# Kernel optimization log

Measured on AMD Instinct MI355X. Metric: run time of the kernel, lower is better.

The kernel has to match this reference:

```python
import jax, jax.numpy as jnp
import numpy as np

EMBED = 1024
HEADS = 16


def setup_inputs() -> dict:
    key = jax.random.key(0)
    k1, k2, k3 = jax.random.split(key, 3)
    B, S, D = 2, 2048, EMBED
    x = jax.random.normal(k1, (B, S, D), dtype=jnp.float32)
    # nn.Linear weights: stored as [out, in]; y = x @ W.T
    w_qkv = jax.random.normal(k2, (3 * D, D), dtype=jnp.float32) * (D ** -0.5)
    w_out = jax.random.normal(k3, (D, D), dtype=jnp.float32) * (D ** -0.5)
    return {"x": x, "w_qkv": w_qkv, "w_out": w_out}


def reference(x, w_qkv, w_out):
    B, S, D = x.shape
    H = HEADS
    hd = D // H
    qkv = x @ w_qkv.T                       # [B, S, 3D]
    q, k, v = jnp.split(qkv, 3, axis=-1)
    # 'b l (head k) -> b head l k'
    def heads(t):
        return t.reshape(B, S, H, hd).transpose(0, 2, 1, 3)
    q, k, v = heads(q), heads(k), heads(v)
    scale = hd ** 0.5
    scores = jnp.einsum('bhqd,bhkd->bhqk', q, k) / scale
    probs = jax.nn.softmax(scores, axis=-1)
    out = jnp.einsum('bhqk,bhkd->bhqd', probs, v)  # [B, H, S, hd]
    out = out.transpose(0, 2, 1, 3).reshape(B, S, D)
    return out @ w_out.T
```

## Files before the change

kernel.cpp:

```cpp
#include <hip/hip_runtime.h>

typedef short short8 __attribute__((ext_vector_type(8)));
typedef short short4v __attribute__((ext_vector_type(4)));
typedef float floatx4 __attribute__((ext_vector_type(4)));
typedef unsigned short ushort_t;

#define EMBED 1024
#define HEADS 16
#define HD 64
#define SEQ 2048
#define BATCH 2
#define QSCALE 0.18033688f

__device__ inline ushort_t f2bf(float f) {
    unsigned int u = __float_as_uint(f);
    u += 0x7fff + ((u >> 16) & 1);
    return (ushort_t)(u >> 16);
}

typedef const __attribute__((address_space(1))) unsigned int* gas_t;
typedef __attribute__((address_space(3))) unsigned int* las_t;
__device__ inline void async_copy16(const ushort_t* g, ushort_t* l) {
    __builtin_amdgcn_global_load_lds((gas_t)g, (las_t)l, 16, 0, 0);
}

__global__ void cast3_kernel(const float* __restrict__ a, ushort_t* __restrict__ oa, int na,
                             const float* __restrict__ b, ushort_t* __restrict__ ob, int nb,
                             const float* __restrict__ c, ushort_t* __restrict__ oc, int nc) {
    int idx = (blockIdx.x * blockDim.x + threadIdx.x) * 4;
    const float* in; ushort_t* out;
    if (idx < na)            { in = a;  out = oa; }
    else if (idx < na + nb)  { in = b;  out = ob; idx -= na; }
    else if (idx < na + nb + nc) { in = c; out = oc; idx -= na + nb; }
    else return;
    float4 f = *(const float4*)(in + idx);
    ushort4 o;
    o.x = f2bf(f.x); o.y = f2bf(f.y); o.z = f2bf(f.z); o.w = f2bf(f.w);
    *(ushort4*)(out + idx) = o;
}

#define BM 128
#define BN 128
#define BK 64

template<int MODE>
__launch_bounds__(256, 3)
__global__ void gemm_bt(const ushort_t* __restrict__ A, const ushort_t* __restrict__ B,
                        float* __restrict__ outF,
                        ushort_t* __restrict__ qb, ushort_t* __restrict__ kb,
                        ushort_t* __restrict__ vtb,
                        int M, int N, int K) {
    __shared__ ushort_t As[BM * BK];
    __shared__ ushort_t Bs[BN * BK];
    const int id   = blockIdx.x;
    const int jj   = id >> 3;
    const int bm   = (id & 7) * 4 + (jj & 3);
    const int bn   = jj >> 2;
    const int t    = threadIdx.x;
    const int lane = t & 63;
    const int wave = t >> 6;
    const int wm   = (wave >> 1) * 64;
    const int wn   = (wave & 1) * 64;
    const int m0   = bm * BM;
    const int n0   = bn * BN;
    const int col  = lane & 15;
    const int quad = lane >> 4;

    const int srow = lane >> 3;
    const int sgr  = (lane & 7) ^ (srow & 7);
    const int slot0 = quad ^ (col & 7);

    floatx4 acc[4][4] = {};

    for (int k0 = 0; k0 < K; k0 += BK) {
        for (int half = 0; half < 4; ++half) {
            int row0 = wave * 32 + half * 8;
            int r = row0 + srow;
            async_copy16(A + (size_t)(m0 + r) * K + k0 + sgr * 8, &As[row0 * BK]);
            async_copy16(B + (size_t)(n0 + r) * K + k0 + sgr * 8, &Bs[row0 * BK]);
        }
        __syncthreads();
        short8 a[2][4], b[2][4];
        for (int i = 0; i < 4; ++i) {
            int base = (wm + i * 16 + col) * BK;
            a[0][i] = *(const short8*)(&As[base + slot0 * 8]);
            a[1][i] = *(const short8*)(&As[base + (slot0 ^ 4) * 8]);
        }
        for (int j = 0; j < 4; ++j) {
            int base = (wn + j * 16 + col) * BK;
            b[0][j] = *(const short8*)(&Bs[base + slot0 * 8]);
            b[1][j] = *(const short8*)(&Bs[base + (slot0 ^ 4) * 8]);
        }
        for (int kk = 0; kk < 2; ++kk)
            for (int i = 0; i < 4; ++i)
                for (int j = 0; j < 4; ++j)
                    acc[i][j] = __builtin_amdgcn_mfma_f32_16x16x32_bf16(a[kk][i], b[kk][j], acc[i][j], 0, 0, 0);
        __syncthreads();
    }

    for (int i = 0; i < 4; ++i)
        for (int j = 0; j < 4; ++j) {
            int n = n0 + wn + j * 16 + col;
            int mb = m0 + wm + i * 16 + quad * 4;
            if (MODE == 1) {
                for (int r = 0; r < 4; ++r)
                    outF[(size_t)(mb + r) * N + n] = acc[i][j][r];
            } else {
                int part = n >> 10;
                int within = n & 1023;
                int h = within >> 6, d = within & 63;
                int bb = mb >> 11, s = mb & 2047;
                if (part == 2) {
                    short4v pv;
                    pv.x = (short)f2bf(acc[i][j][0]); pv.y = (short)f2bf(acc[i][j][1]);
                    pv.z = (short)f2bf(acc[i][j][2]); pv.w = (short)f2bf(acc[i][j][3]);
                    *(short4v*)(vtb + (((size_t)bb * HEADS + h) * HD + d) * SEQ + s) = pv;
                } else {
                    ushort_t* dst = (part == 0) ? qb : kb;
                    const float scl = (part == 0) ? QSCALE : 1.0f;
                    for (int r = 0; r < 4; ++r)
                        dst[(((size_t)bb * HEADS + h) * SEQ + s + r) * HD + d] = f2bf(acc[i][j][r] * scl);
                }
            }
        }
}

__launch_bounds__(512, 4)
__global__ void attn_kernel(const ushort_t* __restrict__ qb_, const ushort_t* __restrict__ kb,
                            const ushort_t* __restrict__ vtb, ushort_t* __restrict__ attn) {
    __shared__ __align__(16) ushort_t lds[32768];
    const int id   = blockIdx.x;
    const int jj   = id >> 3;
    const int bh   = (id & 7) * 4 + (jj >> 4);
    const int qblk = jj & 15;
    const int t    = threadIdx.x;
    const int lane = t & 63;
    const int wave = t >> 6;
    const int g    = wave >> 2;
    const int wv   = wave & 3;
    const int col  = lane & 15;
    const int quad = lane >> 4;
    const int q0   = qblk * 128 + wv * 32;
    const int sw   = col & 7;
    const int srow = lane >> 3;
    const int sgr  = lane & 7;

    const ushort_t* Q  = qb_ + (size_t)bh * SEQ * HD;
    const ushort_t* Kp = kb  + (size_t)bh * SEQ * HD;
    const ushort_t* Vt = vtb + (size_t)bh * HD * SEQ;

    ushort_t* Kb0 = &lds[g * 8192];
    ushort_t* Vb0 = &lds[16384 + g * 8192];

    auto stage = [&](int c, int buf) {
        int kt = c << 6;
        #pragma unroll
        for (int inst = 0; inst < 2; ++inst) {
            int row0 = wv * 16 + inst * 8;
            int r = row0 + srow;
            async_copy16(Kp + (size_t)(kt + r) * HD + (sgr ^ (r & 7)) * 8,
                         Kb0 + buf * 4096 + row0 * 64);
            async_copy16(Vt + (size_t)r * SEQ + kt + (sgr ^ (r & 7)) * 8,
                         Vb0 + buf * 4096 + row0 * 64);
        }
    };

    short8 qf[2][2];
    #pragma unroll
    for (int qt = 0; qt < 2; ++qt) {
        qf[qt][0] = *(const short8*)(Q + (size_t)(q0 + qt * 16 + col) * HD + quad * 8);
        qf[qt][1] = *(const short8*)(Q + (size_t)(q0 + qt * 16 + col) * HD + 32 + quad * 8);
    }

    floatx4 acc[2][4] = {};
    float lsum[2] = {0.f, 0.f};

    stage(g, 0);
    __syncthreads();

    for (int i = 0; i < 16; ++i) {
        const int cur = i & 1;
        if (i < 15) stage(2 * (i + 1) + g, cur ^ 1);
        const ushort_t* Kc = Kb0 + cur * 4096;
        const ushort_t* Vc = Vb0 + cur * 4096;

        #pragma unroll
        for (int h = 0; h < 2; ++h) {
            short8 kf[2][2];
            short4v vf[4][2];
            #pragma unroll
            for (int nl = 0; nl < 2; ++nl) {
                int row = (2 * h + nl) * 16 + col;
                kf[nl][0] = *(const short8*)(Kc + row * 64 + ((quad ^ sw) * 8));
                kf[nl][1] = *(const short8*)(Kc + row * 64 + (((4 + quad) ^ sw) * 8));
            }
            #pragma unroll
            for (int dt = 0; dt < 4; ++dt)
                #pragma unroll
                for (int kl = 0; kl < 2; ++kl) {
                    int ks = h * 2 + kl;
                    int row = dt * 16 + col;
                    int slot = (ks * 2 + (quad >> 1)) ^ sw;
                    vf[dt][kl] = *(const short4v*)(Vc + row * 64 + slot * 8 + (quad & 1) * 4);
                }
            #pragma unroll
            for (int qt = 0; qt < 2; ++qt)
                #pragma unroll
                for (int nl = 0; nl < 2; ++nl) {
                    floatx4 z = {};
                    z = __builtin_amdgcn_mfma_f32_16x16x32_bf16(kf[nl][0], qf[qt][0], z, 0, 0, 0);
                    z = __builtin_amdgcn_mfma_f32_16x16x32_bf16(kf[nl][1], qf[qt][1], z, 0, 0, 0);
                    unsigned u0 = __float_as_uint(__builtin_amdgcn_exp2f(z[0]));
                    unsigned u1 = __float_as_uint(__builtin_amdgcn_exp2f(z[1]));
                    unsigned u2 = __float_as_uint(__builtin_amdgcn_exp2f(z[2]));
                    unsigned u3 = __float_as_uint(__builtin_amdgcn_exp2f(z[3]));
                    lsum[qt] += (__uint_as_float(u0 & 0xffff0000u) + __uint_as_float(u1 & 0xffff0000u))
                              + (__uint_as_float(u2 & 0xffff0000u) + __uint_as_float(u3 & 0xffff0000u));
                    uint2 pk;
                    pk.x = __builtin_amdgcn_perm(u1, u0, 0x07060302u);
                    pk.y = __builtin_amdgcn_perm(u3, u2, 0x07060302u);
                    short4v pb = *(short4v*)&pk;
                    #pragma unroll
                    for (int dt = 0; dt < 4; ++dt)
                        acc[qt][dt] = __builtin_amdgcn_mfma_f32_16x16x16bf16_1k(
                            vf[dt][nl], pb, acc[qt][dt], 0, 0, 0);
                }
        }
        __syncthreads();
    }

    float* fs = (float*)lds;
    const int slot = (wave * 64 + lane) * 20;
    floatx4 accK[4];
    float lsK;
    if (g == 0) {
        #pragma unroll
        for (int d = 0; d < 4; ++d) { *(floatx4*)(&fs[slot + d * 4]) = acc[1][d]; accK[d] = acc[0][d]; }
        fs[slot + 16] = lsum[1]; lsK = lsum[0];
    } else {
        #pragma unroll
        for (int d = 0; d < 4; ++d) { *(floatx4*)(&fs[slot + d * 4]) = acc[0][d]; accK[d] = acc[1][d]; }
        fs[slot + 16] = lsum[0]; lsK = lsum[1];
    }
    __syncthreads();
    const int pslot = ((wave ^ 4) * 64 + lane) * 20;
    #pragma unroll
    for (int d = 0; d < 4; ++d)
        accK[d] += *(const floatx4*)(&fs[pslot + d * 4]);
    float s = lsK + fs[pslot + 16];
    s += __shfl_xor(s, 16);
    s += __shfl_xor(s, 32);
    float inv = 1.0f / s;

    int b = bh >> 4, hh = bh & 15;
    int row = q0 + g * 16 + col;
    #pragma unroll
    for (int dt = 0; dt < 4; ++dt) {
        short4v o;
        o.x = (short)f2bf(accK[dt][0] * inv);
        o.y = (short)f2bf(accK[dt][1] * inv);
        o.z = (short)f2bf(accK[dt][2] * inv);
        o.w = (short)f2bf(accK[dt][3] * inv);
        *(short4v*)(attn + ((size_t)b * SEQ + row) * EMBED + hh * HD + dt * 16 + quad * 4) = o;
    }
}

extern "C" void kernel_launch(void* const* d_in, const int* in_sizes, int n_in,
                              void* d_out, int out_size, void* d_ws, size_t ws_size,
                              hipStream_t stream) {
    const float* x     = (const float*)d_in[0];
    const float* w_qkv = (const float*)d_in[1];
    const float* w_out = (const float*)d_in[2];
    float* out = (float*)d_out;

    char* ws = (char*)d_ws;
    size_t off = 0;
    ushort_t* x_bf    = (ushort_t*)(ws + off); off += (size_t)BATCH * SEQ * EMBED * 2;
    ushort_t* wqkv_bf = (ushort_t*)(ws + off); off += (size_t)3 * EMBED * EMBED * 2;
    ushort_t* wout_bf = (ushort_t*)(ws + off); off += (size_t)EMBED * EMBED * 2;
    ushort_t* q_buf   = (ushort_t*)(ws + off); off += (size_t)BATCH * HEADS * SEQ * HD * 2;
    ushort_t* k_buf   = (ushort_t*)(ws + off); off += (size_t)BATCH * HEADS * SEQ * HD * 2;
    ushort_t* vt_buf  = (ushort_t*)(ws + off); off += (size_t)BATCH * HEADS * SEQ * HD * 2;
    ushort_t* attn_bf = (ushort_t*)(ws + off); off += (size_t)BATCH * SEQ * EMBED * 2;

    int n_x = BATCH * SEQ * EMBED, n_wq = 3 * EMBED * EMBED, n_wo = EMBED * EMBED;
    int n_all = n_x + n_wq + n_wo;
    cast3_kernel<<<n_all / 1024, 256, 0, stream>>>(x, x_bf, n_x, w_qkv, wqkv_bf, n_wq,
                                                   w_out, wout_bf, n_wo);

    gemm_bt<0><<<768, 256, 0, stream>>>(
        x_bf, wqkv_bf, nullptr, q_buf, k_buf, vt_buf, BATCH * SEQ, 3 * EMBED, EMBED);

    attn_kernel<<<512, 512, 0, stream>>>(q_buf, k_buf, vt_buf, attn_bf);

    gemm_bt<1><<<256, 256, 0, stream>>>(
        attn_bf, wout_bf, out, nullptr, nullptr, nullptr, BATCH * SEQ, EMBED, EMBED);
}
```

Measured before the change: 181.3 us.

## Split attention keys across four waves and narrow output GEMM tile

```diff
diff --git a/kernel.cpp b/kernel.cpp
--- a/kernel.cpp
+++ b/kernel.cpp
@@ -40,10 +40,9 @@
 }
 
 #define BM 128
-#define BN 128
 #define BK 64
 
-template<int MODE>
+template<int MODE, int TBN>
 __launch_bounds__(256, 3)
 __global__ void gemm_bt(const ushort_t* __restrict__ A, const ushort_t* __restrict__ B,
                         float* __restrict__ outF,
@@ -51,7 +50,7 @@
                         ushort_t* __restrict__ vtb,
                         int M, int N, int K) {
     __shared__ ushort_t As[BM * BK];
-    __shared__ ushort_t Bs[BN * BK];
+    __shared__ ushort_t Bs[TBN * BK];
     const int id   = blockIdx.x;
     const int jj   = id >> 3;
     const int bm   = (id & 7) * 4 + (jj & 3);
@@ -60,46 +59,51 @@
     const int lane = t & 63;
     const int wave = t >> 6;
     const int wm   = (wave >> 1) * 64;
-    const int wn   = (wave & 1) * 64;
+    const int wn   = (wave & 1) * (TBN / 2);
     const int m0   = bm * BM;
-    const int n0   = bn * BN;
+    const int n0   = bn * TBN;
     const int col  = lane & 15;
     const int quad = lane >> 4;
+    constexpr int NJ = TBN / 32;
 
     const int srow = lane >> 3;
     const int sgr  = (lane & 7) ^ (srow & 7);
     const int slot0 = quad ^ (col & 7);
 
-    floatx4 acc[4][4] = {};
+    floatx4 acc[4][NJ] = {};
 
     for (int k0 = 0; k0 < K; k0 += BK) {
         for (int half = 0; half < 4; ++half) {
             int row0 = wave * 32 + half * 8;
             int r = row0 + srow;
             async_copy16(A + (size_t)(m0 + r) * K + k0 + sgr * 8, &As[row0 * BK]);
+        }
+        for (int half = 0; half < TBN / 32; ++half) {
+            int row0 = wave * (TBN / 4) + half * 8;
+            int r = row0 + srow;
             async_copy16(B + (size_t)(n0 + r) * K + k0 + sgr * 8, &Bs[row0 * BK]);
         }
         __syncthreads();
-        short8 a[2][4], b[2][4];
+        short8 a[2][4], b[2][NJ];
         for (int i = 0; i < 4; ++i) {
             int base = (wm + i * 16 + col) * BK;
             a[0][i] = *(const short8*)(&As[base + slot0 * 8]);
             a[1][i] = *(const short8*)(&As[base + (slot0 ^ 4) * 8]);
         }
-        for (int j = 0; j < 4; ++j) {
+        for (int j = 0; j < NJ; ++j) {
             int base = (wn + j * 16 + col) * BK;
             b[0][j] = *(const short8*)(&Bs[base + slot0 * 8]);
             b[1][j] = *(const short8*)(&Bs[base + (slot0 ^ 4) * 8]);
         }
         for (int kk = 0; kk < 2; ++kk)
             for (int i = 0; i < 4; ++i)
-                for (int j = 0; j < 4; ++j)
+                for (int j = 0; j < NJ; ++j)
                     acc[i][j] = __builtin_amdgcn_mfma_f32_16x16x32_bf16(a[kk][i], b[kk][j], acc[i][j], 0, 0, 0);
         __syncthreads();
     }
 
     for (int i = 0; i < 4; ++i)
-        for (int j = 0; j < 4; ++j) {
+        for (int j = 0; j < NJ; ++j) {
             int n = n0 + wn + j * 16 + col;
             int mb = m0 + wm + i * 16 + quad * 4;
             if (MODE == 1) {
@@ -125,22 +129,22 @@
         }
 }
 
-__launch_bounds__(512, 4)
+__launch_bounds__(256, 4)
 __global__ void attn_kernel(const ushort_t* __restrict__ qb_, const ushort_t* __restrict__ kb,
                             const ushort_t* __restrict__ vtb, ushort_t* __restrict__ attn) {
-    __shared__ __align__(16) ushort_t lds[32768];
+    __shared__ __align__(16) ushort_t lds[16384];
     const int id   = blockIdx.x;
     const int jj   = id >> 3;
-    const int bh   = (id & 7) * 4 + (jj >> 4);
-    const int qblk = jj & 15;
+    const int bh   = (id & 7) * 4 + (jj >> 5);
+    const int qblk = jj & 31;
     const int t    = threadIdx.x;
     const int lane = t & 63;
-    const int wave = t >> 6;
-    const int g    = wave >> 2;
-    const int wv   = wave & 3;
+    const int g    = t >> 6;
     const int col  = lane & 15;
     const int quad = lane >> 4;
-    const int q0   = qblk * 128 + wv * 32;
+    const int qh   = quad >> 1;
+    const int qb2  = quad & 1;
+    const int q0   = qblk * 64;
     const int sw   = col & 7;
     const int srow = lane >> 3;
     const int sgr  = lane & 7;
@@ -149,119 +153,146 @@
     const ushort_t* Kp = kb  + (size_t)bh * SEQ * HD;
     const ushort_t* Vt = vtb + (size_t)bh * HD * SEQ;
 
-    ushort_t* Kb0 = &lds[g * 8192];
-    ushort_t* Vb0 = &lds[16384 + g * 8192];
+    ushort_t* Klds = lds;
+    ushort_t* Vlds = lds + 8192;
 
     auto stage = [&](int c, int buf) {
         int kt = c << 6;
         #pragma unroll
         for (int inst = 0; inst < 2; ++inst) {
-            int row0 = wv * 16 + inst * 8;
+            int row0 = g * 16 + inst * 8;
             int r = row0 + srow;
             async_copy16(Kp + (size_t)(kt + r) * HD + (sgr ^ (r & 7)) * 8,
-                         Kb0 + buf * 4096 + row0 * 64);
+                         Klds + buf * 4096 + row0 * 64);
             async_copy16(Vt + (size_t)r * SEQ + kt + (sgr ^ (r & 7)) * 8,
-                         Vb0 + buf * 4096 + row0 * 64);
+                         Vlds + buf * 4096 + row0 * 64);
         }
     };
 
-    short8 qf[2][2];
+    short8 qf[4][2];
     #pragma unroll
-    for (int qt = 0; qt < 2; ++qt) {
+    for (int qt = 0; qt < 4; ++qt) {
         qf[qt][0] = *(const short8*)(Q + (size_t)(q0 + qt * 16 + col) * HD + quad * 8);
         qf[qt][1] = *(const short8*)(Q + (size_t)(q0 + qt * 16 + col) * HD + 32 + quad * 8);
     }
 
-    floatx4 acc[2][4] = {};
-    float lsum[2] = {0.f, 0.f};
-
-    stage(g, 0);
+    floatx4 acc[4][4] = {};
+    float lsum[4] = {0.f, 0.f, 0.f, 0.f};
+
+    stage(0, 0);
     __syncthreads();
 
-    for (int i = 0; i < 16; ++i) {
+    for (int i = 0; i < 32; ++i) {
         const int cur = i & 1;
-        if (i < 15) stage(2 * (i + 1) + g, cur ^ 1);
-        const ushort_t* Kc = Kb0 + cur * 4096;
-        const ushort_t* Vc = Vb0 + cur * 4096;
-
+        if (i < 31) stage(i + 1, cur ^ 1);
+        const ushort_t* Kc = Klds + cur * 4096;
+        const ushort_t* Vc = Vlds + cur * 4096;
+
+        short8 kf0 = *(const short8*)(Kc + (g * 16 + col) * 64 + ((quad ^ sw) * 8));
+        short8 kf1 = *(const short8*)(Kc + (g * 16 + col) * 64 + (((4 + quad) ^ sw) * 8));
+        short4v vf[4];
         #pragma unroll
-        for (int h = 0; h < 2; ++h) {
-            short8 kf[2][2];
-            short4v vf[4][2];
-            #pragma unroll
-            for (int nl = 0; nl < 2; ++nl) {
-                int row = (2 * h + nl) * 16 + col;
-                kf[nl][0] = *(const short8*)(Kc + row * 64 + ((quad ^ sw) * 8));
-                kf[nl][1] = *(const short8*)(Kc + row * 64 + (((4 + quad) ^ sw) * 8));
-            }
+        for (int dt = 0; dt < 4; ++dt)
+            vf[dt] = *(const short4v*)(Vc + (dt * 16 + col) * 64
+                                       + (((g * 2 + qh) ^ sw) * 8) + qb2 * 4);
+        #pragma unroll
+        for (int qt = 0; qt < 4; ++qt) {
+            floatx4 z = {};
+            __builtin_amdgcn_s_setprio(1);
+            z = __builtin_amdgcn_mfma_f32_16x16x32_bf16(kf0, qf[qt][0], z, 0, 0, 0);
+            z = __builtin_amdgcn_mfma_f32_16x16x32_bf16(kf1, qf[qt][1], z, 0, 0, 0);
+            __builtin_amdgcn_s_setprio(0);
+            unsigned u0 = __float_as_uint(__builtin_amdgcn_exp2f(z[0]));
+            unsigned u1 = __float_as_uint(__builtin_amdgcn_exp2f(z[1]));
+            unsigned u2 = __float_as_uint(__builtin_amdgcn_exp2f(z[2]));
+            unsigned u3 = __float_as_uint(__builtin_amdgcn_exp2f(z[3]));
+            lsum[qt] += (__uint_as_float(u0 & 0xffff0000u) + __uint_as_float(u1 & 0xffff0000u))
+                      + (__uint_as_float(u2 & 0xffff0000u) + __uint_as_float(u3 & 0xffff0000u));
+            uint2 pk;
+            pk.x = __builtin_amdgcn_perm(u1, u0, 0x07060302u);
+            pk.y = __builtin_amdgcn_perm(u3, u2, 0x07060302u);
+            short4v pb = *(short4v*)&pk;
+            __builtin_amdgcn_s_setprio(1);
             #pragma unroll
             for (int dt = 0; dt < 4; ++dt)
+                acc[qt][dt] = __builtin_amdgcn_mfma_f32_16x16x16bf16_1k(
+                    vf[dt], pb, acc[qt][dt], 0, 0, 0);
+            __builtin_amdgcn_s_setprio(0);
+        }
+        __syncthreads();
+    }
+
+    float* fs = (float*)lds;
+    #pragma unroll
+    for (int half = 0; half < 2; ++half) {
+        if (g & 1) {
+            int ws = ((g >> 1) * 64 + lane) * 36;
+            #pragma unroll
+            for (int qt = 0; qt < 2; ++qt) {
                 #pragma unroll
-                for (int kl = 0; kl < 2; ++kl) {
-                    int ks = h * 2 + kl;
-                    int row = dt * 16 + col;
-                    int slot = (ks * 2 + (quad >> 1)) ^ sw;
-                    vf[dt][kl] = *(const short4v*)(Vc + row * 64 + slot * 8 + (quad & 1) * 4);
-                }
-            #pragma unroll
-            for (int qt = 0; qt < 2; ++qt)
+                for (int dt = 0; dt < 4; ++dt)
+                    *(floatx4*)&fs[ws + (qt * 4 + dt) * 4] = acc[half * 2 + qt][dt];
+                fs[ws + 32 + qt] = lsum[half * 2 + qt];
+            }
+        }
+        __syncthreads();
+        if (!(g & 1)) {
+            int ps = ((g >> 1) * 64 + lane) * 36;
+            #pragma unroll
+            for (int qt = 0; qt < 2; ++qt) {
                 #pragma unroll
-                for (int nl = 0; nl < 2; ++nl) {
-                    floatx4 z = {};
-                    z = __builtin_amdgcn_mfma_f32_16x16x32_bf16(kf[nl][0], qf[qt][0], z, 0, 0, 0);
-                    z = __builtin_amdgcn_mfma_f32_16x16x32_bf16(kf[nl][1], qf[qt][1], z, 0, 0, 0);
-                    unsigned u0 = __float_as_uint(__builtin_amdgcn_exp2f(z[0]));
-                    unsigned u1 = __float_as_uint(__builtin_amdgcn_exp2f(z[1]));
-                    unsigned u2 = __float_as_uint(__builtin_amdgcn_exp2f(z[2]));
-                    unsigned u3 = __float_as_uint(__builtin_amdgcn_exp2f(z[3]));
-                    lsum[qt] += (__uint_as_float(u0 & 0xffff0000u) + __uint_as_float(u1 & 0xffff0000u))
-                              + (__uint_as_float(u2 & 0xffff0000u) + __uint_as_float(u3 & 0xffff0000u));
-                    uint2 pk;
-                    pk.x = __builtin_amdgcn_perm(u1, u0, 0x07060302u);
-                    pk.y = __builtin_amdgcn_perm(u3, u2, 0x07060302u);
-                    short4v pb = *(short4v*)&pk;
-                    #pragma unroll
-                    for (int dt = 0; dt < 4; ++dt)
-                        acc[qt][dt] = __builtin_amdgcn_mfma_f32_16x16x16bf16_1k(
-                            vf[dt][nl], pb, acc[qt][dt], 0, 0, 0);
-                }
-        }
-        __syncthreads();
-    }
-
-    float* fs = (float*)lds;
-    const int slot = (wave * 64 + lane) * 20;
-    floatx4 accK[4];
-    float lsK;
+                for (int dt = 0; dt < 4; ++dt)
+                    acc[half * 2 + qt][dt] += *(const floatx4*)&fs[ps + (qt * 4 + dt) * 4];
+                lsum[half * 2 + qt] += fs[ps + 32 + qt];
+            }
+        }
+        __syncthreads();
+    }
+    #pragma unroll
+    for (int half = 0; half < 2; ++half) {
+        if (g == 2) {
+            int ws = lane * 36;
+            #pragma unroll
+            for (int qt = 0; qt < 2; ++qt) {
+                #pragma unroll
+                for (int dt = 0; dt < 4; ++dt)
+                    *(floatx4*)&fs[ws + (qt * 4 + dt) * 4] = acc[half * 2 + qt][dt];
+                fs[ws + 32 + qt] = lsum[half * 2 + qt];
+            }
+        }
+        __syncthreads();
+        if (g == 0) {
+            int ps = lane * 36;
+            #pragma unroll
+            for (int qt = 0; qt < 2; ++qt) {
+                #pragma unroll
+                for (int dt = 0; dt < 4; ++dt)
+                    acc[half * 2 + qt][dt] += *(const floatx4*)&fs[ps + (qt * 4 + dt) * 4];
+                lsum[half * 2 + qt] += fs[ps + 32 + qt];
+            }
+        }
+        __syncthreads();
+    }
+
     if (g == 0) {
+        int b = bh >> 4, hh = bh & 15;
         #pragma unroll
-        for (int d = 0; d < 4; ++d) { *(floatx4*)(&fs[slot + d * 4]) = acc[1][d]; accK[d] = acc[0][d]; }
-        fs[slot + 16] = lsum[1]; lsK = lsum[0];
-    } else {
-        #pragma unroll
-        for (int d = 0; d < 4; ++d) { *(floatx4*)(&fs[slot + d * 4]) = acc[0][d]; accK[d] = acc[1][d]; }
-        fs[slot + 16] = lsum[0]; lsK = lsum[1];
-    }
-    __syncthreads();
-    const int pslot = ((wave ^ 4) * 64 + lane) * 20;
-    #pragma unroll
-    for (int d = 0; d < 4; ++d)
-        accK[d] += *(const floatx4*)(&fs[pslot + d * 4]);
-    float s = lsK + fs[pslot + 16];
-    s += __shfl_xor(s, 16);
-    s += __shfl_xor(s, 32);
-    float inv = 1.0f / s;
-
-    int b = bh >> 4, hh = bh & 15;
-    int row = q0 + g * 16 + col;
-    #pragma unroll
-    for (int dt = 0; dt < 4; ++dt) {
-        short4v o;
-        o.x = (short)f2bf(accK[dt][0] * inv);
-        o.y = (short)f2bf(accK[dt][1] * inv);
-        o.z = (short)f2bf(accK[dt][2] * inv);
-        o.w = (short)f2bf(accK[dt][3] * inv);
-        *(short4v*)(attn + ((size_t)b * SEQ + row) * EMBED + hh * HD + dt * 16 + quad * 4) = o;
+        for (int qt = 0; qt < 4; ++qt) {
+            float s = lsum[qt];
+            s += __shfl_xor(s, 16);
+            s += __shfl_xor(s, 32);
+            float inv = 1.0f / s;
+            int row = q0 + qt * 16 + col;
+            #pragma unroll
+            for (int dt = 0; dt < 4; ++dt) {
+                short4v o;
+                o.x = (short)f2bf(acc[qt][dt][0] * inv);
+                o.y = (short)f2bf(acc[qt][dt][1] * inv);
+                o.z = (short)f2bf(acc[qt][dt][2] * inv);
+                o.w = (short)f2bf(acc[qt][dt][3] * inv);
+                *(short4v*)(attn + ((size_t)b * SEQ + row) * EMBED + hh * HD + dt * 16 + quad * 4) = o;
+            }
+        }
     }
 }
 
@@ -288,11 +319,11 @@
     cast3_kernel<<<n_all / 1024, 256, 0, stream>>>(x, x_bf, n_x, w_qkv, wqkv_bf, n_wq,
                                                    w_out, wout_bf, n_wo);
 
-    gemm_bt<0><<<768, 256, 0, stream>>>(
+    gemm_bt<0, 128><<<768, 256, 0, stream>>>(
         x_bf, wqkv_bf, nullptr, q_buf, k_buf, vt_buf, BATCH * SEQ, 3 * EMBED, EMBED);
 
-    attn_kernel<<<512, 512, 0, stream>>>(q_buf, k_buf, vt_buf, attn_bf);
-
-    gemm_bt<1><<<256, 256, 0, stream>>>(
+    attn_kernel<<<1024, 256, 0, stream>>>(q_buf, k_buf, vt_buf, attn_bf);
+
+    gemm_bt<1, 64><<<512, 256, 0, stream>>>(
         attn_bf, wout_bf, out, nullptr, nullptr, nullptr, BATCH * SEQ, EMBED, EMBED);
 }
```

After: 226.1 us. +24.7%, slower.
